# Optimization experiments

Hardware: AMD Instinct MI355X
Metric: run time of the kernel (lower is better)

The kernel has to match this reference:

```python
import jax, jax.numpy as jnp
import numpy as np

B, N, M = 4, 4096, 4096  # samples, pred pts/sample, target pts/sample
LOSS_WEIGHT = 1.0


def setup_inputs() -> dict:
    key = jax.random.key(0)
    k1, k2, k3 = jax.random.split(key, 3)
    pred_pc = jax.random.normal(k1, (B * N, 3), dtype=jnp.float32)
    target = jax.random.normal(k2, (B * M, 3), dtype=jnp.float32)
    label = jax.random.randint(k3, (B * N,), 0, 2)  # binary keep-mask per pred point
    nums = jnp.full((B,), N, dtype=jnp.int32)        # uniform ragged sizes (static for jit)
    dense_nums = jnp.full((B,), M, dtype=jnp.int32)
    return {"pred_pc": pred_pc, "target": target, "label": label,
            "nums": nums, "dense_nums": dense_nums}


def reference(pred_pc, target, label, nums, dense_nums):
    b = nums.shape[0]
    p = pred_pc.reshape(b, -1, 3)      # [B,N,3]
    t = target.reshape(b, -1, 3)       # [B,M,3]
    mask = (label.reshape(b, -1) == 1) # [B,N] valid pred points

    # squared pairwise distances via |p|^2 + |t|^2 - 2 p.t  -> [B,N,M]
    pn = jnp.sum(p * p, axis=-1)
    tn = jnp.sum(t * t, axis=-1)
    d = pn[:, :, None] + tn[:, None, :] - 2.0 * jnp.einsum('bnd,bmd->bnm', p, t)
    d = jnp.maximum(d, 0.0)

    # pred -> target: min over M, L1 (sqrt before mean), masked mean over valid preds
    d1 = jnp.sqrt(jnp.min(d, axis=2))                              # [B,N]
    cnt = jnp.maximum(jnp.sum(mask, axis=1), 1)
    m1 = jnp.sum(jnp.where(mask, d1, 0.0), axis=1) / cnt           # [B]

    # target -> pred: min over valid pred points only (invalid rows masked to +big)
    BIG = jnp.float32(1e10)
    d2 = jnp.sqrt(jnp.min(jnp.where(mask[:, :, None], d, BIG), axis=1))  # [B,M]
    m2 = jnp.mean(d2, axis=1)                                      # [B]

    per_sample = 0.5 * (m1 + m2)   # ChamferDistanceL1: (d1.mean()+d2.mean())/2
    return jnp.mean(per_sample) * LOSS_WEIGHT
```

## Files before the change

### kernel.cpp

```cpp
#include <hip/hip_runtime.h>

#define TPB   256
#define QPT   8
#define SPLIT 32
#define RTPB  256
#define CPB   8

typedef float f32x2 __attribute__((ext_vector_type(2)));


__global__ void __launch_bounds__(TPB) nn_kernel(
    const float* __restrict__ pred,
    const float* __restrict__ target,
    const int*   __restrict__ label,
    float* __restrict__ minsplit,
    unsigned int* __restrict__ counter,
    int B, int N, int M, int natmax, int stride)
{
    __shared__ float xs[TPB], ys[TPB], zs[TPB], ws[TPB];

    if (blockIdx.x == 0 && blockIdx.y == 0 && blockIdx.z == 0 && threadIdx.x == 0) {
        *counter = 0u;
    }

    const int dir = blockIdx.z;
    const float* __restrict__ A  = dir ? target : pred;
    const float* __restrict__ Bp = dir ? pred   : target;
    const int NA = dir ? M : N;
    const int NB = dir ? N : M;
    const int* __restrict__ labB = dir ? label : nullptr;

    const int natiles = (NA + TPB * QPT - 1) / (TPB * QPT);
    const int b  = blockIdx.x / natmax;
    const int at = blockIdx.x - b * natmax;
    if (at >= natiles) return;

    const size_t abase = (size_t)b * NA;

    float px[QPT], py[QPT], pz[QPT], pn[QPT];
    f32x2 best2[QPT];
#pragma unroll
    for (int q = 0; q < QPT; ++q) {
        int a = at * (TPB * QPT) + q * TPB + threadIdx.x;
        int idx = (a < NA) ? a : 0;
        const float* sp = A + (abase + idx) * 3;
        px[q] = sp[0];
        py[q] = sp[1];
        pz[q] = sp[2];
        pn[q] = fmaf(px[q], px[q], fmaf(py[q], py[q], pz[q] * pz[q]));
        best2[q] = (f32x2){3.0e38f, 3.0e38f};
    }

    const int slen = (NB + SPLIT - 1) / SPLIT;
    const int sbeg = blockIdx.y * slen;
    const int send = min(sbeg + slen, NB);
    const size_t bbase = (size_t)b * NB;

    for (int c = sbeg; c < send; c += TPB) {
        const int cnt = min(send - c, TPB);
        if (threadIdx.x < cnt) {
            int m = c + threadIdx.x;
            const float* sp = Bp + (bbase + m) * 3;
            float x = sp[0], y = sp[1], z = sp[2];
            float tn = fmaf(x, x, fmaf(y, y, z * z));
            if (labB != nullptr && labB[bbase + m] != 1) {
                x = 0.0f; y = 0.0f; z = 0.0f; tn = 1.0e10f;
            }
            xs[threadIdx.x] = -2.0f * x;
            ys[threadIdx.x] = -2.0f * y;
            zs[threadIdx.x] = -2.0f * z;
            ws[threadIdx.x] = tn;
        }
        __syncthreads();

        const int npair = cnt >> 1;
#pragma unroll 4
        for (int jp = 0; jp < npair; ++jp) {
            f32x2 tx = *reinterpret_cast<const f32x2*>(&xs[2 * jp]);
            f32x2 ty = *reinterpret_cast<const f32x2*>(&ys[2 * jp]);
            f32x2 tz = *reinterpret_cast<const f32x2*>(&zs[2 * jp]);
            f32x2 tw = *reinterpret_cast<const f32x2*>(&ws[2 * jp]);
#pragma unroll
            for (int q = 0; q < QPT; ++q) {
                f32x2 vx = {px[q], px[q]};
                f32x2 vy = {py[q], py[q]};
                f32x2 vz = {pz[q], pz[q]};
                f32x2 v = __builtin_elementwise_fma(vx, tx,
                          __builtin_elementwise_fma(vy, ty,
                          __builtin_elementwise_fma(vz, tz, tw)));
                best2[q] = __builtin_elementwise_min(best2[q], v);
            }
        }
        if (cnt & 1) {
            float tx = xs[cnt - 1], ty = ys[cnt - 1], tz = zs[cnt - 1], tw = ws[cnt - 1];
#pragma unroll
            for (int q = 0; q < QPT; ++q) {
                float v = fmaf(px[q], tx, fmaf(py[q], ty, fmaf(pz[q], tz, tw)));
                best2[q].x = fminf(best2[q].x, v);
            }
        }
        __syncthreads();
    }

    float* out = minsplit + (((size_t)dir * B + b) * SPLIT + blockIdx.y) * stride;
#pragma unroll
    for (int q = 0; q < QPT; ++q) {
        int a = at * (TPB * QPT) + q * TPB + threadIdx.x;
        if (a < NA) {
            float best = fminf(best2[q].x, best2[q].y);
            out[a] = fmaxf(best + pn[q], 0.0f);
        }
    }
}

__device__ __forceinline__ void block_reduce2(float& s, float& cc, float* red) {
    int tid = threadIdx.x;
    red[tid] = s;
    red[RTPB + tid] = cc;
    __syncthreads();
    for (int o = RTPB / 2; o > 0; o >>= 1) {
        if (tid < o) {
            red[tid]        += red[tid + o];
            red[RTPB + tid] += red[RTPB + tid + o];
        }
        __syncthreads();
    }
    s  = red[0];
    cc = red[RTPB];
    __syncthreads();
}

__global__ void __launch_bounds__(RTPB) reduce_final_kernel(
    const float* __restrict__ minsplit,
    const int* __restrict__ label,
    float* __restrict__ pS, float* __restrict__ pC,
    unsigned int* __restrict__ counter,
    float* __restrict__ out,
    int B, int N, int M, int stride, int nblocks)
{
    __shared__ float red[2 * RTPB];
    const int r = blockIdx.x;

    const int dir = r / (B * CPB);
    const int rem = r - dir * (B * CPB);
    const int b   = rem / CPB;
    const int ch  = rem - b * CPB;
    const int NA  = dir ? M : N;
    const int qc  = (NA + CPB - 1) / CPB;
    const int qpt = (qc + RTPB - 1) / RTPB;

    const float* base = minsplit + ((size_t)(dir * B + b) * SPLIT) * stride;

    float s = 0.0f, cc = 0.0f;
    for (int k = 0; k < qpt; ++k) {
        int q = ch * qc + k * RTPB + threadIdx.x;
        if (q < min((ch + 1) * qc, NA)) {
            float m = base[q];
#pragma unroll 8
            for (int sp = 1; sp < SPLIT; ++sp) {
                m = fminf(m, base[(size_t)sp * stride + q]);
            }
            if (dir == 0) {
                if (label[(size_t)b * N + q] == 1) { s += sqrtf(m); cc += 1.0f; }
            } else {
                s += sqrtf(m);
            }
        }
    }

    block_reduce2(s, cc, red);

    __shared__ unsigned int is_last;
    if (threadIdx.x == 0) {
        atomicExch(&pS[r], s);
        atomicExch(&pC[r], cc);
        __threadfence();
        unsigned int old = atomicAdd(counter, 1u);
        is_last = (old == (unsigned int)(nblocks - 1)) ? 1u : 0u;
    }
    __syncthreads();

    if (is_last) {
        __shared__ float sS[2 * 64], sC[2 * 64];
        for (int i = threadIdx.x; i < nblocks; i += RTPB) {
            sS[i] = atomicAdd(&pS[i], 0.0f);
            sC[i] = atomicAdd(&pC[i], 0.0f);
        }
        __syncthreads();
        if (threadIdx.x == 0) {
            float acc = 0.0f;
            for (int bb = 0; bb < B; ++bb) {
                float S1 = 0.0f, C1 = 0.0f, S2 = 0.0f;
                for (int i = 0; i < CPB; ++i) {
                    S1 += sS[bb * CPB + i];
                    C1 += sC[bb * CPB + i];
                    S2 += sS[B * CPB + bb * CPB + i];
                }
                float m1 = S1 / fmaxf(C1, 1.0f);
                float m2 = S2 / (float)M;
                acc += 0.5f * (m1 + m2);
            }
            out[0] = acc / (float)B;
        }
    }
}

extern "C" void kernel_launch(void* const* d_in, const int* in_sizes, int n_in,
                              void* d_out, int out_size, void* d_ws, size_t ws_size,
                              hipStream_t stream) {
    const float* pred   = (const float*)d_in[0];
    const float* target = (const float*)d_in[1];
    const int*   label  = (const int*)  d_in[2];

    const int B = in_sizes[3];
    const int N = in_sizes[2] / B;
    const int M = in_sizes[1] / (3 * B);

    const int stride = (N > M) ? N : M;

    float* minsplit = (float*)d_ws;
    const int nred = 2 * B * CPB;
    float* pS = minsplit + (size_t)2 * B * SPLIT * stride;
    float* pC = pS + nred;
    unsigned int* counter = (unsigned int*)(pC + nred);

    const int nat1 = (N + TPB * QPT - 1) / (TPB * QPT);
    const int nat2 = (M + TPB * QPT - 1) / (TPB * QPT);
    const int natmax = (nat1 > nat2) ? nat1 : nat2;
    dim3 g(B * natmax, SPLIT, 2);
    nn_kernel<<<g, TPB, 0, stream>>>(pred, target, label, minsplit, counter,
                                     B, N, M, natmax, stride);

    reduce_final_kernel<<<nred, RTPB, 0, stream>>>(minsplit, label, pS, pC,
                                                   counter, (float*)d_out,
                                                   B, N, M, stride, nred);
}
```

Before: 30.76 us.

## Fuse nearest-neighbor and reduction kernels via per-block flags and spin-waits

Merges the NN-distance kernel and the reduce/finalize kernel into one launch. Blocks publish completion flags, designated blocks spin-wait on the flags for their sample before doing the split-min and sum reduction, and block 0 waits on the reduction flags, writes the final scalar, then clears all flags for the next call. The aim is to remove the second launch and the gap between kernels. The cost is spin-waiting, which can deadlock if waiting blocks are resident while the blocks they wait on are not, plus reliance on the workspace flags starting at zero. The chunk count per sample also goes from 8 to 16 and a min-occupancy hint is added to the launch bounds.

```diff
diff --git a/kernel.cpp b/kernel.cpp
--- a/kernel.cpp
+++ b/kernel.cpp
@@ -3,190 +3,216 @@
 #define TPB   256
 #define QPT   8
 #define SPLIT 32
-#define RTPB  256
-#define CPB   8
+#define CPB   16
+#define MAXRED 256
+#define MAGIC 0x5AD00D5Au
 
 typedef float f32x2 __attribute__((ext_vector_type(2)));
 
 
-__global__ void __launch_bounds__(TPB) nn_kernel(
+__device__ __forceinline__ void block_reduce2(float& s, float& cc, float* red) {
+    int tid = threadIdx.x;
+    red[tid] = s;
+    red[TPB + tid] = cc;
+    __syncthreads();
+    for (int o = TPB / 2; o > 0; o >>= 1) {
+        if (tid < o) {
+            red[tid]       += red[tid + o];
+            red[TPB + tid] += red[TPB + tid + o];
+        }
+        __syncthreads();
+    }
+    s  = red[0];
+    cc = red[TPB];
+    __syncthreads();
+}
+
+__global__ void __launch_bounds__(TPB, 2) fused_kernel(
     const float* __restrict__ pred,
     const float* __restrict__ target,
     const int*   __restrict__ label,
     float* __restrict__ minsplit,
-    unsigned int* __restrict__ counter,
+    float* __restrict__ pS, float* __restrict__ pC,
+    unsigned int* __restrict__ nnflag,
+    unsigned int* __restrict__ redflag,
+    float* __restrict__ out,
     int B, int N, int M, int natmax, int stride)
 {
     __shared__ float xs[TPB], ys[TPB], zs[TPB], ws[TPB];
-
-    if (blockIdx.x == 0 && blockIdx.y == 0 && blockIdx.z == 0 && threadIdx.x == 0) {
-        *counter = 0u;
-    }
-
-    const int dir = blockIdx.z;
-    const float* __restrict__ A  = dir ? target : pred;
-    const float* __restrict__ Bp = dir ? pred   : target;
-    const int NA = dir ? M : N;
-    const int NB = dir ? N : M;
-    const int* __restrict__ labB = dir ? label : nullptr;
-
-    const int natiles = (NA + TPB * QPT - 1) / (TPB * QPT);
-    const int b  = blockIdx.x / natmax;
-    const int at = blockIdx.x - b * natmax;
-    if (at >= natiles) return;
-
-    const size_t abase = (size_t)b * NA;
-
-    float px[QPT], py[QPT], pz[QPT], pn[QPT];
-    f32x2 best2[QPT];
-#pragma unroll
-    for (int q = 0; q < QPT; ++q) {
-        int a = at * (TPB * QPT) + q * TPB + threadIdx.x;
-        int idx = (a < NA) ? a : 0;
-        const float* sp = A + (abase + idx) * 3;
-        px[q] = sp[0];
-        py[q] = sp[1];
-        pz[q] = sp[2];
-        pn[q] = fmaf(px[q], px[q], fmaf(py[q], py[q], pz[q] * pz[q]));
-        best2[q] = (f32x2){3.0e38f, 3.0e38f};
-    }
-
-    const int slen = (NB + SPLIT - 1) / SPLIT;
-    const int sbeg = blockIdx.y * slen;
-    const int send = min(sbeg + slen, NB);
-    const size_t bbase = (size_t)b * NB;
-
-    for (int c = sbeg; c < send; c += TPB) {
-        const int cnt = min(send - c, TPB);
-        if (threadIdx.x < cnt) {
-            int m = c + threadIdx.x;
-            const float* sp = Bp + (bbase + m) * 3;
-            float x = sp[0], y = sp[1], z = sp[2];
-            float tn = fmaf(x, x, fmaf(y, y, z * z));
-            if (labB != nullptr && labB[bbase + m] != 1) {
-                x = 0.0f; y = 0.0f; z = 0.0f; tn = 1.0e10f;
-            }
-            xs[threadIdx.x] = -2.0f * x;
-            ys[threadIdx.x] = -2.0f * y;
-            zs[threadIdx.x] = -2.0f * z;
-            ws[threadIdx.x] = tn;
-        }
-        __syncthreads();
-
-        const int npair = cnt >> 1;
+    __shared__ float red[2 * TPB];
+
+    const int bid = blockIdx.x;
+    const int per_dir = B * natmax * SPLIT;
+
+    {
+        const int dir = bid / per_dir;
+        const int r1  = bid - dir * per_dir;
+        const int b   = r1 / (natmax * SPLIT);
+        const int r2  = r1 - b * (natmax * SPLIT);
+        const int at  = r2 / SPLIT;
+        const int sp  = r2 - at * SPLIT;
+
+        const float* __restrict__ A  = dir ? target : pred;
+        const float* __restrict__ Bp = dir ? pred   : target;
+        const int NA = dir ? M : N;
+        const int NB = dir ? N : M;
+        const int* __restrict__ labB = dir ? label : nullptr;
+
+        const int natiles = (NA + TPB * QPT - 1) / (TPB * QPT);
+        if (at < natiles) {
+            const size_t abase = (size_t)b * NA;
+
+            float px[QPT], py[QPT], pz[QPT], pn[QPT];
+            f32x2 best2[QPT];
+#pragma unroll
+            for (int q = 0; q < QPT; ++q) {
+                int a = at * (TPB * QPT) + q * TPB + threadIdx.x;
+                int idx = (a < NA) ? a : 0;
+                const float* spq = A + (abase + idx) * 3;
+                px[q] = spq[0];
+                py[q] = spq[1];
+                pz[q] = spq[2];
+                pn[q] = fmaf(px[q], px[q], fmaf(py[q], py[q], pz[q] * pz[q]));
+                best2[q] = (f32x2){3.0e38f, 3.0e38f};
+            }
+
+            const int slen = (NB + SPLIT - 1) / SPLIT;
+            const int sbeg = sp * slen;
+            const int send = min(sbeg + slen, NB);
+            const size_t bbase = (size_t)b * NB;
+
+            for (int c = sbeg; c < send; c += TPB) {
+                const int cnt = min(send - c, TPB);
+                if (threadIdx.x < cnt) {
+                    int m = c + threadIdx.x;
+                    const float* spm = Bp + (bbase + m) * 3;
+                    float x = spm[0], y = spm[1], z = spm[2];
+                    float tn = fmaf(x, x, fmaf(y, y, z * z));
+                    if (labB != nullptr && labB[bbase + m] != 1) {
+                        x = 0.0f; y = 0.0f; z = 0.0f; tn = 1.0e10f;
+                    }
+                    xs[threadIdx.x] = -2.0f * x;
+                    ys[threadIdx.x] = -2.0f * y;
+                    zs[threadIdx.x] = -2.0f * z;
+                    ws[threadIdx.x] = tn;
+                }
+                __syncthreads();
+
+                const int npair = cnt >> 1;
 #pragma unroll 4
-        for (int jp = 0; jp < npair; ++jp) {
-            f32x2 tx = *reinterpret_cast<const f32x2*>(&xs[2 * jp]);
-            f32x2 ty = *reinterpret_cast<const f32x2*>(&ys[2 * jp]);
-            f32x2 tz = *reinterpret_cast<const f32x2*>(&zs[2 * jp]);
-            f32x2 tw = *reinterpret_cast<const f32x2*>(&ws[2 * jp]);
+                for (int jp = 0; jp < npair; ++jp) {
+                    f32x2 tx = *reinterpret_cast<const f32x2*>(&xs[2 * jp]);
+                    f32x2 ty = *reinterpret_cast<const f32x2*>(&ys[2 * jp]);
+                    f32x2 tz = *reinterpret_cast<const f32x2*>(&zs[2 * jp]);
+                    f32x2 tw = *reinterpret_cast<const f32x2*>(&ws[2 * jp]);
+#pragma unroll
+                    for (int q = 0; q < QPT; ++q) {
+                        f32x2 vx = {px[q], px[q]};
+                        f32x2 vy = {py[q], py[q]};
+                        f32x2 vz = {pz[q], pz[q]};
+                        f32x2 v = __builtin_elementwise_fma(vx, tx,
+                                  __builtin_elementwise_fma(vy, ty,
+                                  __builtin_elementwise_fma(vz, tz, tw)));
+                        best2[q] = __builtin_elementwise_min(best2[q], v);
+                    }
+                }
+                if (cnt & 1) {
+                    float tx = xs[cnt - 1], ty = ys[cnt - 1];
+                    float tz = zs[cnt - 1], tw = ws[cnt - 1];
+#pragma unroll
+                    for (int q = 0; q < QPT; ++q) {
+                        float v = fmaf(px[q], tx, fmaf(py[q], ty, fmaf(pz[q], tz, tw)));
+                        best2[q].x = fminf(best2[q].x, v);
+                    }
+                }
+                __syncthreads();
+            }
+
+            float* o = minsplit + (((size_t)dir * B + b) * SPLIT + sp) * stride;
 #pragma unroll
             for (int q = 0; q < QPT; ++q) {
-                f32x2 vx = {px[q], px[q]};
-                f32x2 vy = {py[q], py[q]};
-                f32x2 vz = {pz[q], pz[q]};
-                f32x2 v = __builtin_elementwise_fma(vx, tx,
-                          __builtin_elementwise_fma(vy, ty,
-                          __builtin_elementwise_fma(vz, tz, tw)));
-                best2[q] = __builtin_elementwise_min(best2[q], v);
-            }
-        }
-        if (cnt & 1) {
-            float tx = xs[cnt - 1], ty = ys[cnt - 1], tz = zs[cnt - 1], tw = ws[cnt - 1];
-#pragma unroll
-            for (int q = 0; q < QPT; ++q) {
-                float v = fmaf(px[q], tx, fmaf(py[q], ty, fmaf(pz[q], tz, tw)));
-                best2[q].x = fminf(best2[q].x, v);
-            }
-        }
-        __syncthreads();
-    }
-
-    float* out = minsplit + (((size_t)dir * B + b) * SPLIT + blockIdx.y) * stride;
-#pragma unroll
-    for (int q = 0; q < QPT; ++q) {
-        int a = at * (TPB * QPT) + q * TPB + threadIdx.x;
-        if (a < NA) {
-            float best = fminf(best2[q].x, best2[q].y);
-            out[a] = fmaxf(best + pn[q], 0.0f);
-        }
-    }
-}
-
-__device__ __forceinline__ void block_reduce2(float& s, float& cc, float* red) {
-    int tid = threadIdx.x;
-    red[tid] = s;
-    red[RTPB + tid] = cc;
-    __syncthreads();
-    for (int o = RTPB / 2; o > 0; o >>= 1) {
-        if (tid < o) {
-            red[tid]        += red[tid + o];
-            red[RTPB + tid] += red[RTPB + tid + o];
-        }
-        __syncthreads();
-    }
-    s  = red[0];
-    cc = red[RTPB];
-    __syncthreads();
-}
-
-__global__ void __launch_bounds__(RTPB) reduce_final_kernel(
-    const float* __restrict__ minsplit,
-    const int* __restrict__ label,
-    float* __restrict__ pS, float* __restrict__ pC,
-    unsigned int* __restrict__ counter,
-    float* __restrict__ out,
-    int B, int N, int M, int stride, int nblocks)
-{
-    __shared__ float red[2 * RTPB];
-    const int r = blockIdx.x;
-
-    const int dir = r / (B * CPB);
-    const int rem = r - dir * (B * CPB);
-    const int b   = rem / CPB;
-    const int ch  = rem - b * CPB;
-    const int NA  = dir ? M : N;
-    const int qc  = (NA + CPB - 1) / CPB;
-    const int qpt = (qc + RTPB - 1) / RTPB;
-
-    const float* base = minsplit + ((size_t)(dir * B + b) * SPLIT) * stride;
-
-    float s = 0.0f, cc = 0.0f;
-    for (int k = 0; k < qpt; ++k) {
-        int q = ch * qc + k * RTPB + threadIdx.x;
-        if (q < min((ch + 1) * qc, NA)) {
-            float m = base[q];
+                int a = at * (TPB * QPT) + q * TPB + threadIdx.x;
+                if (a < NA) {
+                    float best = fminf(best2[q].x, best2[q].y);
+                    o[a] = fmaxf(best + pn[q], 0.0f);
+                }
+            }
+        }
+    }
+
+    __threadfence();
+    if (threadIdx.x == 0) {
+        atomicExch(&nnflag[bid], MAGIC);
+    }
+
+    const int rstride = (natmax * SPLIT) / CPB;
+    const int nred = 2 * B * CPB;
+
+    if ((bid % rstride) == 0) {
+        const int rid = bid / rstride;
+        const int dir = rid / (B * CPB);
+        const int rem = rid - dir * (B * CPB);
+        const int b   = rem / CPB;
+        const int ch  = rem - b * CPB;
+        const int NA  = dir ? M : N;
+
+        const int fbase  = dir * per_dir + b * (natmax * SPLIT);
+        const int nflags = natmax * SPLIT;
+        for (int i = threadIdx.x; i < nflags; i += TPB) {
+            while (__hip_atomic_load(&nnflag[fbase + i], __ATOMIC_ACQUIRE,
+                                     __HIP_MEMORY_SCOPE_AGENT) != MAGIC) {
+                __builtin_amdgcn_s_sleep(2);
+            }
+        }
+        __syncthreads();
+
+        const int qc  = (NA + CPB - 1) / CPB;
+        const int qpt = (qc + TPB - 1) / TPB;
+        const float* base = minsplit + ((size_t)(dir * B + b) * SPLIT) * stride;
+
+        float s = 0.0f, cc = 0.0f;
+        for (int k = 0; k < qpt; ++k) {
+            int q = ch * qc + k * TPB + threadIdx.x;
+            if (q < min((ch + 1) * qc, NA)) {
+                float m = base[q];
 #pragma unroll 8
-            for (int sp = 1; sp < SPLIT; ++sp) {
-                m = fminf(m, base[(size_t)sp * stride + q]);
-            }
-            if (dir == 0) {
-                if (label[(size_t)b * N + q] == 1) { s += sqrtf(m); cc += 1.0f; }
-            } else {
-                s += sqrtf(m);
-            }
-        }
-    }
-
-    block_reduce2(s, cc, red);
-
-    __shared__ unsigned int is_last;
-    if (threadIdx.x == 0) {
-        atomicExch(&pS[r], s);
-        atomicExch(&pC[r], cc);
-        __threadfence();
-        unsigned int old = atomicAdd(counter, 1u);
-        is_last = (old == (unsigned int)(nblocks - 1)) ? 1u : 0u;
-    }
-    __syncthreads();
-
-    if (is_last) {
-        __shared__ float sS[2 * 64], sC[2 * 64];
-        for (int i = threadIdx.x; i < nblocks; i += RTPB) {
+                for (int sp = 1; sp < SPLIT; ++sp) {
+                    m = fminf(m, base[(size_t)sp * stride + q]);
+                }
+                if (dir == 0) {
+                    if (label[(size_t)b * N + q] == 1) { s += sqrtf(m); cc += 1.0f; }
+                } else {
+                    s += sqrtf(m);
+                }
+            }
+        }
+
+        block_reduce2(s, cc, red);
+
+        if (threadIdx.x == 0) {
+            pS[rid] = s;
+            pC[rid] = cc;
+            __threadfence();
+            atomicExch(&redflag[rid], MAGIC);
+        }
+    }
+
+    if (bid == 0) {
+        for (int i = threadIdx.x; i < nred; i += TPB) {
+            while (__hip_atomic_load(&redflag[i], __ATOMIC_ACQUIRE,
+                                     __HIP_MEMORY_SCOPE_AGENT) != MAGIC) {
+                __builtin_amdgcn_s_sleep(2);
+            }
+        }
+        __syncthreads();
+
+        __shared__ float sS[MAXRED], sC[MAXRED];
+        for (int i = threadIdx.x; i < nred; i += TPB) {
             sS[i] = atomicAdd(&pS[i], 0.0f);
             sC[i] = atomicAdd(&pC[i], 0.0f);
         }
         __syncthreads();
+
         if (threadIdx.x == 0) {
             float acc = 0.0f;
             for (int bb = 0; bb < B; ++bb) {
@@ -202,6 +228,10 @@
             }
             out[0] = acc / (float)B;
         }
+        __syncthreads();
+
+        for (int i = threadIdx.x; i < 2 * per_dir; i += TPB) nnflag[i] = 0u;
+        for (int i = threadIdx.x; i < nred; i += TPB)        redflag[i] = 0u;
     }
 }
 
@@ -222,16 +252,15 @@
     const int nred = 2 * B * CPB;
     float* pS = minsplit + (size_t)2 * B * SPLIT * stride;
     float* pC = pS + nred;
-    unsigned int* counter = (unsigned int*)(pC + nred);
-
+    unsigned int* nnflag  = (unsigned int*)(pC + nred);
     const int nat1 = (N + TPB * QPT - 1) / (TPB * QPT);
     const int nat2 = (M + TPB * QPT - 1) / (TPB * QPT);
     const int natmax = (nat1 > nat2) ? nat1 : nat2;
-    dim3 g(B * natmax, SPLIT, 2);
-    nn_kernel<<<g, TPB, 0, stream>>>(pred, target, label, minsplit, counter,
-                                     B, N, M, natmax, stride);
-
-    reduce_final_kernel<<<nred, RTPB, 0, stream>>>(minsplit, label, pS, pC,
-                                                   counter, (float*)d_out,
-                                                   B, N, M, stride, nred);
+    const int nblocks = 2 * B * natmax * SPLIT;
+    unsigned int* redflag = nnflag + nblocks;
+
+    fused_kernel<<<nblocks, TPB, 0, stream>>>(pred, target, label, minsplit,
+                                              pS, pC, nnflag, redflag,
+                                              (float*)d_out,
+                                              B, N, M, natmax, stride);
 }
```

New measurement: 81.08 us. 164% more time.
